# Performance work log

Hardware: AMD Instinct MI355X
Metric: run time of the kernel (lower is better)

## Reference

```python
import jax, jax.numpy as jnp
import numpy as np

HEADS = 4
PK = 32  # patch_kernel


def _starts(size, step, d):
    out = []
    for i in range(0, size + step - d, step):
        out.append(min(i, size - d))
    return np.asarray(out)


def dwconv3(x, w, b=None):
    # depthwise 3x3 conv, NCHW, weight (C,1,3,3)
    y = jax.lax.conv_general_dilated(
        x, w, window_strides=(1, 1), padding=((1, 1), (1, 1)),
        dimension_numbers=("NCHW", "OIHW", "NCHW"), feature_group_count=x.shape[1])
    if b is not None:
        y = y + b[None, :, None, None]
    return y


def conv1(x, w):
    # 1x1 conv as channel matmul, weight (O, C)
    return jnp.einsum("bchw,oc->bohw", x, w)


def partition(x, step, d):
    # overlapping windows, matching local_partition (i outer, j inner)
    b, c, h, w = x.shape
    sh = _starts(h, step, d)
    sw = _starts(w, step, d)
    ridx = sh[:, None] + np.arange(d)            # (nh, d)
    cidx = sw[:, None] + np.arange(d)            # (nw, d)
    xw = x[:, :, ridx, :]                        # (b, c, nh, d, w)
    xw = xw[:, :, :, :, cidx]                    # (b, c, nh, d, nw, d)
    xw = jnp.transpose(xw, (0, 2, 4, 1, 3, 5))   # (b, nh, nw, c, d, d)
    return xw.reshape(b, len(sh) * len(sw), c, d, d)


def reverse(shape, win, step, d):
    # overlap-add + count-based averaging, matching local_reverse
    b, c, h, w = shape
    sh = _starts(h, step, d)
    sw = _starts(w, step, d)
    nh, nw = len(sh), len(sw)
    ridx = (sh[:, None] + np.arange(d)).reshape(nh, 1, d, 1)
    cidx = (sw[:, None] + np.arange(d)).reshape(1, nw, 1, d)
    win6 = win.reshape(b, nh, nw, c, d, d).transpose(0, 3, 1, 2, 4, 5)  # (b,c,nh,nw,d,d)
    out = jnp.zeros(shape, win.dtype).at[:, :, ridx, cidx].add(win6)
    cnt = jnp.zeros((h, w), win.dtype).at[ridx, cidx].add(1.0)
    return out / cnt[None, None]


def setup_inputs() -> dict:
    key = jax.random.key(0)
    ks = jax.random.split(key, 9)
    b, dim, Hs, Hx = 2, 128, 62, 248
    s = 0.05
    return {
        "x": jax.random.normal(ks[0], (b, dim, Hx, Hx), jnp.float32),
        "sp": jax.random.normal(ks[1], (b, dim, Hs, Hs), jnp.float32),
        "w_pos": jax.random.normal(ks[2], (dim, 1, 3, 3), jnp.float32) * s,
        "b_pos": jax.random.normal(ks[3], (dim,), jnp.float32) * s,
        "w_q": jax.random.normal(ks[4], (dim, dim), jnp.float32) * s,
        "w_qdw": jax.random.normal(ks[5], (dim, 1, 3, 3), jnp.float32) * s,
        "w_kv": jax.random.normal(ks[6], (2 * dim, dim), jnp.float32) * s,
        "w_kvdw": jax.random.normal(ks[7], (2 * dim, 1, 3, 3), jnp.float32) * s,
        "w_out": jax.random.normal(ks[8], (dim, dim), jnp.float32) * s,
    }


def reference(x, sp, w_pos, b_pos, w_q, w_qdw, w_kv, w_kvdw, w_out):
    p1, p2 = PK, PK // 4               # 32, 8
    s1, s2 = p1 - p1 // 4, p2 - p2 // 4  # 24, 6
    x = x + dwconv3(x, w_pos, b_pos)
    sp = sp + dwconv3(sp, w_pos, b_pos)
    q = dwconv3(conv1(sp, w_q), w_qdw)      # (b, c, Hs, Ws)
    kv = dwconv3(conv1(x, w_kv), w_kvdw)    # (b, 2c, Hx, Wx)
    qw = partition(q, s2, p2)               # (b, n, c, 8, 8)
    kvw = partition(kv, s1, p1)             # (b, n, 2c, 32, 32)
    kw, vw = jnp.split(kvw, 2, axis=2)
    b, n, c = qw.shape[0], qw.shape[1], qw.shape[2]
    hd = c // HEADS

    def to_heads(t, d):  # 'b n (head c) dh dw -> (b n) head (dh dw) c'
        return t.reshape(b * n, HEADS, hd, d * d).transpose(0, 1, 3, 2)

    qh, kh, vh = to_heads(qw, p2), to_heads(kw, p1), to_heads(vw, p1)
    attn = jax.nn.softmax(jnp.einsum("bhqc,bhkc->bhqk", qh, kh) * (hd ** -0.5), axis=-1)
    out = jnp.einsum("bhqk,bhkc->bhqc", attn, vh)
    out = out.transpose(0, 1, 3, 2).reshape(b, n, c, p2, p2)
    out = reverse(sp.shape, out, s2, p2)
    return conv1(out, w_out)
```

## Files before the change

kernel.cpp:

```cpp
#include <hip/hip_runtime.h>
#include <cstdint>

#define HS 62
#define HX 248
#define HXW (HX * HX)
#define HSW (HS * HS)
#define HXP 256
#define HXWP (HX * HXP)

typedef __attribute__((ext_vector_type(8))) short bf16x8;
typedef __attribute__((ext_vector_type(4))) float f32x4;
typedef __attribute__((ext_vector_type(2))) float f32x2;

static __device__ __forceinline__ unsigned short f2bf(float f) {
  uint32_t u = __builtin_bit_cast(uint32_t, f);
  u += 0x7fff + ((u >> 16) & 1);
  return (unsigned short)(u >> 16);
}
static __device__ __forceinline__ float bf2f(unsigned short u) {
  uint32_t x = (uint32_t)u << 16;
  return __builtin_bit_cast(float, x);
}
static __device__ __forceinline__ float bflo(uint32_t u) {
  return __builtin_bit_cast(float, u << 16);
}
static __device__ __forceinline__ float bfhi(uint32_t u) {
  return __builtin_bit_cast(float, u & 0xffff0000u);
}

static __device__ __forceinline__ void pkfma(f32x2& acc, f32x2 a, f32x2 b) {
  asm("v_pk_fma_f32 %0, %1, %2, %0" : "+v"(acc) : "v"(a), "v"(b));
}
static __device__ __forceinline__ uint32_t cvtpk(float lo, float hi) {
  uint32_t r;
  asm("v_cvt_pk_bf16_f32 %0, %1, %2" : "=v"(r) : "v"(lo), "v"(hi));
  return r;
}
static __device__ __forceinline__ f32x2 unp(uint32_t u) {
  f32x2 r;
  r.x = __builtin_bit_cast(float, u << 16);
  r.y = __builtin_bit_cast(float, u & 0xffff0000u);
  return r;
}

__global__ void dwconv3_kernel(const float* __restrict__ x, const float* __restrict__ w,
                               const float* __restrict__ bias, float* __restrict__ y,
                               int C, int H, int W, int total, int residual) {
  int i = blockIdx.x * 256 + threadIdx.x;
  if (i >= total) return;
  int wx = i % W;
  int t = i / W;
  int hy = t % H;
  int bc = t / H;
  int c = bc % C;
  const float* xb = x + (size_t)bc * H * W;
  const float* wc = w + c * 9;
  float s = bias ? bias[c] : 0.0f;
  for (int di = -1; di <= 1; di++) {
    int h2 = hy + di;
    if (h2 < 0 || h2 >= H) continue;
    for (int dj = -1; dj <= 1; dj++) {
      int w2 = wx + dj;
      if (w2 < 0 || w2 >= W) continue;
      s += xb[(size_t)h2 * W + w2] * wc[(di + 1) * 3 + (dj + 1)];
    }
  }
  if (residual) s += xb[(size_t)hy * W + wx];
  y[i] = s;
}

__global__ __launch_bounds__(256) void dwconv8x2_bf16_kernel(
    const float* __restrict__ x, const float* __restrict__ w,
    const float* __restrict__ bias, unsigned short* __restrict__ y, int total) {
  int i = blockIdx.x * 256 + threadIdx.x;
  if (i >= total) return;
  int wq = (i % 31) * 8;
  int t = i / 31;
  int hp = t % 124;
  int bc = t / 124;
  int c = bc & 127;
  int hy = hp * 2;
  const float* xb = x + (size_t)bc * HXW;
  const float* wc = w + c * 9;
  float bv = bias[c];

  float rm1[10], r0[10], r1[10], r2[10];
  auto loadrow = [&](int h2, float (&r)[10]) {
    const float* row = xb + (size_t)h2 * HX + wq;
    float4 a = *(const float4*)row;
    float4 b2 = *(const float4*)(row + 4);
    r[1] = a.x;  r[2] = a.y;  r[3] = a.z;  r[4] = a.w;
    r[5] = b2.x; r[6] = b2.y; r[7] = b2.z; r[8] = b2.w;
    r[0] = (wq > 0) ? row[-1] : 0.0f;
    r[9] = (wq + 8 < HX) ? row[8] : 0.0f;
  };
  loadrow((hy > 0) ? hy - 1 : 0, rm1);
  loadrow(hy, r0);
  loadrow(hy + 1, r1);
  loadrow((hy + 2 < HX) ? hy + 2 : HX - 1, r2);
  if (hp == 0) {
#pragma unroll
    for (int k = 0; k < 10; k++) rm1[k] = 0.0f;
  }
  if (hp == 123) {
#pragma unroll
    for (int k = 0; k < 10; k++) r2[k] = 0.0f;
  }

  float w0 = wc[0], w1 = wc[1], w2 = wc[2];
  float w3 = wc[3], w4 = wc[4], w5 = wc[5];
  float w6 = wc[6], w7 = wc[7], w8 = wc[8];

  float o0[8], o1[8];
#pragma unroll
  for (int k = 0; k < 8; k++) {
    float s = bv;
    s += w0 * rm1[k]; s += w1 * rm1[k + 1]; s += w2 * rm1[k + 2];
    s += w3 * r0[k];  s += w4 * r0[k + 1];  s += w5 * r0[k + 2];
    s += w6 * r1[k];  s += w7 * r1[k + 1];  s += w8 * r1[k + 2];
    o0[k] = s + r0[k + 1];
    float u = bv;
    u += w0 * r0[k]; u += w1 * r0[k + 1]; u += w2 * r0[k + 2];
    u += w3 * r1[k]; u += w4 * r1[k + 1]; u += w5 * r1[k + 2];
    u += w6 * r2[k]; u += w7 * r2[k + 1]; u += w8 * r2[k + 2];
    o1[k] = u + r1[k + 1];
  }
  uint4 d0, d1;
  d0.x = cvtpk(o0[0], o0[1]); d0.y = cvtpk(o0[2], o0[3]);
  d0.z = cvtpk(o0[4], o0[5]); d0.w = cvtpk(o0[6], o0[7]);
  d1.x = cvtpk(o1[0], o1[1]); d1.y = cvtpk(o1[2], o1[3]);
  d1.z = cvtpk(o1[4], o1[5]); d1.w = cvtpk(o1[6], o1[7]);
  unsigned short* yb = y + (size_t)bc * HXW + (size_t)hy * HX + wq;
  *(uint4*)yb = d0;
  *(uint4*)(yb + HX) = d1;
}

__global__ void cvt_bf16_kernel(const float* __restrict__ src, unsigned short* __restrict__ dst,
                                int n) {
  int i = blockIdx.x * 256 + threadIdx.x;
  if (i < n) dst[i] = f2bf(src[i]);
}

__global__ void dwconv_q_kernel(const float* __restrict__ x, const float* __restrict__ w,
                                unsigned short* __restrict__ qn, int total) {
  int i = blockIdx.x * 256 + threadIdx.x;
  if (i >= total) return;
  int wx = i % HS;
  int t = i / HS;
  int hy = t % HS;
  int bc = t / HS;
  int c = bc & 127;
  int b = bc >> 7;
  const float* xb = x + (size_t)bc * HSW;
  const float* wc = w + c * 9;
  float s = 0.0f;
  for (int di = -1; di <= 1; di++) {
    int h2 = hy + di;
    if (h2 < 0 || h2 >= HS) continue;
    for (int dj = -1; dj <= 1; dj++) {
      int w2 = wx + dj;
      if (w2 < 0 || w2 >= HS) continue;
      s += xb[(size_t)h2 * HS + w2] * wc[(di + 1) * 3 + (dj + 1)];
    }
  }
  qn[((size_t)(b * HSW + hy * HS + wx)) * 128 + c] = f2bf(s * 0.17677669529663688f);
}

__global__ __launch_bounds__(256) void conv1_kv_mfma_kernel(
    const unsigned short* __restrict__ xpb,
    const unsigned short* __restrict__ wkb,
    unsigned short* __restrict__ y) {
  int b = blockIdx.y;
  int p0 = blockIdx.x * 64;
  int tid = threadIdx.x;
  int wave = tid >> 6, lane = tid & 63, quad = lane >> 4, l15 = lane & 15;
  __shared__ __align__(16) unsigned short bufA[64 * 136];
  __shared__ __align__(16) unsigned short bufW[64 * 136];

  {
    int c = tid >> 1, half = tid & 1;
    const unsigned short* src = xpb + ((size_t)(b * 128 + c)) * HXW + p0 + half * 32;
#pragma unroll
    for (int j = 0; j < 8; j++) {
      uint2 v = *(const uint2*)(src + j * 4);
      int px = half * 32 + j * 4;
      bufA[(px + 0) * 136 + c] = (unsigned short)(v.x & 0xffff);
      bufA[(px + 1) * 136 + c] = (unsigned short)(v.x >> 16);
      bufA[(px + 2) * 136 + c] = (unsigned short)(v.y & 0xffff);
      bufA[(px + 3) * 136 + c] = (unsigned short)(v.y >> 16);
    }
  }
  __syncthreads();
  bf16x8 A[4];
#pragma unroll
  for (int kb = 0; kb < 4; kb++)
    A[kb] = __builtin_bit_cast(bf16x8,
        *(const uint4*)&bufA[(wave * 16 + l15) * 136 + kb * 32 + quad * 8]);

  const f32x4 zf = {0.f, 0.f, 0.f, 0.f};
#pragma unroll 1
  for (int h = 0; h < 2; h++) {
#pragma unroll 1
    for (int oq = 0; oq < 2; oq++) {
      __syncthreads();
      {
        int orow = tid >> 2;
        int cseg = (tid & 3) * 32;
        const unsigned short* src = wkb + (size_t)(h * 128 + oq * 64 + orow) * 128 + cseg;
        unsigned short* dst = &bufW[orow * 136 + cseg];
        *(uint4*)(dst)      = *(const uint4*)(src);
        *(uint4*)(dst + 8)  = *(const uint4*)(src + 8);
        *(uint4*)(dst + 16) = *(const uint4*)(src + 16);
        *(uint4*)(dst + 24) = *(const uint4*)(src + 24);
      }
      __syncthreads();
#pragma unroll
      for (int ot = 0; ot < 4; ot++) {
        const unsigned short* wrow = &bufW[(ot * 16 + l15) * 136 + quad * 8];
        f32x4 D = zf;
        D = __builtin_amdgcn_mfma_f32_16x16x32_bf16(A[0], __builtin_bit_cast(bf16x8, *(const uint4*)(wrow)),      D, 0, 0, 0);
        D = __builtin_amdgcn_mfma_f32_16x16x32_bf16(A[1], __builtin_bit_cast(bf16x8, *(const uint4*)(wrow + 32)), D, 0, 0, 0);
        D = __builtin_amdgcn_mfma_f32_16x16x32_bf16(A[2], __builtin_bit_cast(bf16x8, *(const uint4*)(wrow + 64)), D, 0, 0, 0);
        D = __builtin_amdgcn_mfma_f32_16x16x32_bf16(A[3], __builtin_bit_cast(bf16x8, *(const uint4*)(wrow + 96)), D, 0, 0, 0);
#pragma unroll
        for (int r = 0; r < 4; r++)
          bufA[(wave * 16 + quad * 4 + r) * 136 + (oq * 4 + ot) * 16 + l15] = f2bf(D[r]);
      }
    }
    __syncthreads();
    {
      int px = tid >> 2, og = (tid & 3) * 32;
      const uint4* srcp = (const uint4*)&bufA[px * 136 + og];
      uint4* dstp = (uint4*)(y + ((size_t)b * HXW + p0 + px) * 256 + h * 128 + og);
#pragma unroll
      for (int j = 0; j < 4; j++) dstp[j] = srcp[j];
    }
  }
}

template <bool VT, bool VB>
static __device__ __forceinline__ void dwkv_rowpair(
    const unsigned short* __restrict__ rm1, const unsigned short* __restrict__ r0,
    const unsigned short* __restrict__ r1, const unsigned short* __restrict__ r2,
    const f32x2 (&wp)[9], int px0, f32x2 (&a0)[8], f32x2 (&a1)[8]) {
  const f32x2 z2 = {0.f, 0.f};
#pragma unroll
  for (int p = 0; p < 8; p++) { a0[p] = z2; a1[p] = z2; }
#pragma unroll
  for (int j = 0; j < 10; j++) {
    int xcol = px0 - 1 + j;
    int xc = xcol;
    if (j == 0) xc = (xcol < 0) ? 0 : xcol;
    if (j == 9) xc = (xcol > HX - 1) ? HX - 1 : xcol;
    size_t off = (size_t)xc * 256;
    uint32_t um1 = 0, u0, u1, u2 = 0;
    u0 = *(const uint32_t*)(r0 + off);
    u1 = *(const uint32_t*)(r1 + off);
    if constexpr (VT) um1 = *(const uint32_t*)(rm1 + off);
    if constexpr (VB) u2 = *(const uint32_t*)(r2 + off);
    if (j == 0 || j == 9) {
      bool oob = (j == 0) ? (xcol < 0) : (xcol > HX - 1);
      if (oob) { um1 = 0u; u0 = 0u; u1 = 0u; u2 = 0u; }
    }
    f32x2 dm1, d0 = unp(u0), d1 = unp(u1), d2;
    if constexpr (VT) dm1 = unp(um1);
    if constexpr (VB) d2 = unp(u2);
    if (j <= 7) {
      if constexpr (VT) pkfma(a0[j], wp[0], dm1);
      pkfma(a0[j], wp[3], d0);
      pkfma(a0[j], wp[6], d1);
      pkfma(a1[j], wp[0], d0);
      pkfma(a1[j], wp[3], d1);
      if constexpr (VB) pkfma(a1[j], wp[6], d2);
    }
    if (j >= 1 && j <= 8) {
      if constexpr (VT) pkfma(a0[j - 1], wp[1], dm1);
      pkfma(a0[j - 1], wp[4], d0);
      pkfma(a0[j - 1], wp[7], d1);
      pkfma(a1[j - 1], wp[1], d0);
      pkfma(a1[j - 1], wp[4], d1);
      if constexpr (VB) pkfma(a1[j - 1], wp[7], d2);
    }
    if (j >= 2) {
      if constexpr (VT) pkfma(a0[j - 2], wp[2], dm1);
      pkfma(a0[j - 2], wp[5], d0);
      pkfma(a0[j - 2], wp[8], d1);
      pkfma(a1[j - 2], wp[2], d0);
      pkfma(a1[j - 2], wp[5], d1);
      if constexpr (VB) pkfma(a1[j - 2], wp[8], d2);
    }
  }
}

#define VTS 72
#define VTROW (128 * VTS + 16)

__global__ __launch_bounds__(512) __attribute__((amdgpu_waves_per_eu(4)))
void dwconv_kv_kernel(const unsigned short* __restrict__ tkv,
                      const float* __restrict__ w,
                      unsigned short* __restrict__ kT,
                      unsigned short* __restrict__ vv) {
  int fid = blockIdx.x;
  int xcd = fid & 7, slot = fid >> 3;
  int gi = xcd * 62 + slot;
  int strip = gi / 124;
  int g = gi % 124;
  int b = blockIdx.y;
  int x0 = strip * 64;
  int tid = threadIdx.x;
  int cl = tid & 127;
  int pg = tid >> 7;
  int ch0 = cl * 2;
  int hy0 = g * 2;

  f32x2 wp[9];
#pragma unroll
  for (int t = 0; t < 9; t++) {
    wp[t].x = w[ch0 * 9 + t];
    wp[t].y = w[(ch0 + 1) * 9 + t];
  }

  __shared__ __align__(16) unsigned short vt[2 * VTROW];

  const unsigned short* r0 = tkv + (size_t)b * HXW * 256 + (size_t)hy0 * (HX * 256) + ch0;
  const unsigned short* r1 = r0 + HX * 256;
  const unsigned short* rm1 = r0 - HX * 256;
  const unsigned short* r2 = r1 + HX * 256;
  bool isK = (cl < 64);
  int c0 = ch0 - 128;

#pragma unroll 1
  for (int half = 0; half < 2; half++) {
    int px0 = x0 + pg * 16 + half * 8;
    if (px0 < HX) {
      f32x2 a0[8], a1[8];
      if (g == 0)        dwkv_rowpair<false, true >(rm1, r0, r1, r2, wp, px0, a0, a1);
      else if (g == 123) dwkv_rowpair<true,  false>(rm1, r0, r1, r2, wp, px0, a0, a1);
      else               dwkv_rowpair<true,  true >(rm1, r0, r1, r2, wp, px0, a0, a1);

      if (isK) {
        unsigned short* kb0 = kT + ((size_t)b * HXW + (size_t)hy0 * HX + px0) * 128 + ch0;
        unsigned short* kb1 = kb0 + (size_t)HX * 128;
#pragma unroll
        for (int p = 0; p < 8; p++) {
          *(uint32_t*)(kb0 + (size_t)p * 128) = cvtpk(a0[p].x, a0[p].y);
          *(uint32_t*)(kb1 + (size_t)p * 128) = cvtpk(a1[p].x, a1[p].y);
        }
      } else {
        int pxr = pg * 16 + half * 8;
        unsigned short* v0 = vt + c0 * VTS + pxr;
        unsigned short* v1 = v0 + VTS;
        uint2 d;
        d.x = cvtpk(a0[0].x, a0[1].x); d.y = cvtpk(a0[2].x, a0[3].x);
        *(uint2*)(v0) = d;
        d.x = cvtpk(a0[4].x, a0[5].x); d.y = cvtpk(a0[6].x, a0[7].x);
        *(uint2*)(v0 + 4) = d;
        d.x = cvtpk(a0[0].y, a0[1].y); d.y = cvtpk(a0[2].y, a0[3].y);
        *(uint2*)(v1) = d;
        d.x = cvtpk(a0[4].y, a0[5].y); d.y = cvtpk(a0[6].y, a0[7].y);
        *(uint2*)(v1 + 4) = d;
        d.x = cvtpk(a1[0].x, a1[1].x); d.y = cvtpk(a1[2].x, a1[3].x);
        *(uint2*)(v0 + VTROW) = d;
        d.x = cvtpk(a1[4].x, a1[5].x); d.y = cvtpk(a1[6].x, a1[7].x);
        *(uint2*)(v0 + VTROW + 4) = d;
        d.x = cvtpk(a1[0].y, a1[1].y); d.y = cvtpk(a1[2].y, a1[3].y);
        *(uint2*)(v1 + VTROW) = d;
        d.x = cvtpk(a1[4].y, a1[5].y); d.y = cvtpk(a1[6].y, a1[7].y);
        *(uint2*)(v1 + VTROW + 4) = d;
      }
    }
  }
  __syncthreads();
  {
    int ch = tid >> 2;
    int row = (tid >> 1) & 1;
    int ph = (tid & 1) * 32;
    const unsigned short* srcv = vt + row * VTROW + ch * VTS + ph;
    unsigned short* dst = vv + (size_t)(b * 128 + ch) * HXWP + (size_t)(hy0 + row) * HXP + x0 + ph;
#pragma unroll
    for (int j = 0; j < 4; j++)
      *(uint4*)(dst + j * 8) = *(const uint4*)(srcv + j * 8);
  }
}

template <int O>
__global__ __launch_bounds__(256) void conv1_kernel(const float* __restrict__ x,
                                                    const float* __restrict__ w,
                                                    float* __restrict__ y, int HW) {
  constexpr int K = 128;
  constexpr int BK = 32;
  __shared__ __align__(16) float ws_s[BK][64];
  __shared__ __align__(16) float xs_s[BK][64];
  int b = blockIdx.z;
  int o0 = blockIdx.y * 64;
  int p0 = blockIdx.x * 64;
  const float* xb = x + (size_t)b * K * HW;
  int tx = threadIdx.x & 15;
  int ty = threadIdx.x >> 4;
  float acc[4][4] = {};
  int lo = threadIdx.x >> 2;
  int lk = (threadIdx.x & 3) * 8;
  int lc = threadIdx.x >> 3;
  int lp = (threadIdx.x & 7) * 8;

  for (int k0 = 0; k0 < K; k0 += BK) {
    __syncthreads();
    {
      const float* wp = w + (size_t)(o0 + lo) * K + k0 + lk;
      float4 a = *(const float4*)wp;
      float4 bq = *(const float4*)(wp + 4);
      ws_s[lk + 0][lo] = a.x;  ws_s[lk + 1][lo] = a.y;
      ws_s[lk + 2][lo] = a.z;  ws_s[lk + 3][lo] = a.w;
      ws_s[lk + 4][lo] = bq.x; ws_s[lk + 5][lo] = bq.y;
      ws_s[lk + 6][lo] = bq.z; ws_s[lk + 7][lo] = bq.w;
    }
    {
      int p = p0 + lp;
      const float* xp = xb + (size_t)(k0 + lc) * HW;
      float4 a, bq;
      if (p + 7 < HW) {
        a = *(const float4*)(xp + p);
        bq = *(const float4*)(xp + p + 4);
      } else {
        float tv[8];
#pragma unroll
        for (int j = 0; j < 8; j++) tv[j] = (p + j < HW) ? xp[p + j] : 0.0f;
        a = make_float4(tv[0], tv[1], tv[2], tv[3]);
        bq = make_float4(tv[4], tv[5], tv[6], tv[7]);
      }
      *(float4*)&xs_s[lc][lp] = a;
      *(float4*)&xs_s[lc][lp + 4] = bq;
    }
    __syncthreads();
#pragma unroll
    for (int k = 0; k < BK; k++) {
      float4 wv = *(const float4*)&ws_s[k][ty * 4];
      float4 xv = *(const float4*)&xs_s[k][tx * 4];
      acc[0][0] += wv.x * xv.x; acc[0][1] += wv.x * xv.y; acc[0][2] += wv.x * xv.z; acc[0][3] += wv.x * xv.w;
      acc[1][0] += wv.y * xv.x; acc[1][1] += wv.y * xv.y; acc[1][2] += wv.y * xv.z; acc[1][3] += wv.y * xv.w;
      acc[2][0] += wv.z * xv.x; acc[2][1] += wv.z * xv.y; acc[2][2] += wv.z * xv.z; acc[2][3] += wv.z * xv.w;
      acc[3][0] += wv.w * xv.x; acc[3][1] += wv.w * xv.y; acc[3][2] += wv.w * xv.z; acc[3][3] += wv.w * xv.w;
    }
  }
  int p = p0 + tx * 4;
  float* yb = y + (size_t)b * O * HW + (size_t)(o0 + ty * 4) * HW;
#pragma unroll
  for (int j = 0; j < 4; j++) {
    float* yr = yb + (size_t)j * HW + p;
    if (p + 3 < HW) {
      *(float4*)yr = make_float4(acc[j][0], acc[j][1], acc[j][2], acc[j][3]);
    } else {
#pragma unroll
      for (int e = 0; e < 4; e++) if (p + e < HW) yr[e] = acc[j][e];
    }
  }
}

__global__ __launch_bounds__(512) void attn_mfma_kernel(
    const unsigned short* __restrict__ qn,
    const unsigned short* __restrict__ kT,
    const unsigned short* __restrict__ vp,
    float* __restrict__ o) {
  int n = blockIdx.x, hp = blockIdx.y, b = blockIdx.z;
  int wi = n / 10, wj = n % 10;
  int wave = threadIdx.x >> 6;
  int hd = wave & 1, oct = wave >> 1;
  int h = hp * 2 + hd;
  int lane = threadIdx.x & 63;
  int quad = lane >> 4;
  int l15 = lane & 15;
  int y0 = 24 * wi, x0 = 24 * wj;

  __shared__ __align__(16) unsigned short lds[20480];
  unsigned short* Pw = lds + wave * 2560;

  bf16x8 QB[4];
#pragma unroll
  for (int nt = 0; nt < 4; nt++) {
    int qq = nt * 16 + l15;
    int qy = 6 * wi + (qq >> 3), qx = 6 * wj + (qq & 7);
    QB[nt] = __builtin_bit_cast(bf16x8,
        *(const uint4*)(qn + ((size_t)(b * HSW + qy * HS + qx)) * 128 + h * 32 + quad * 8));
  }

  f32x4 Oacc[2][4];
#pragma unroll
  for (int a = 0; a < 2; a++)
#pragma unroll
    for (int c = 0; c < 4; c++) Oacc[a][c] = f32x4{0.f, 0.f, 0.f, 0.f};
  float lsum[4] = {0.f, 0.f, 0.f, 0.f};

  const unsigned short* kb = kT + (size_t)b * HXW * 128 + h * 32;
  const unsigned short* vb = vp + ((size_t)(b * 128 + h * 32)) * HXWP;
  const f32x4 zf = {0.f, 0.f, 0.f, 0.f};

#define LOADROW(r, K0, K1, V0, V1)                                              \
  {                                                                             \
    int y = y0 + (r);                                                           \
    const unsigned short* krow = kb + ((size_t)(y * HX + x0)) * 128;            \
    K0 = *(const uint4*)(krow + (size_t)l15 * 128 + quad * 8);                  \
    K1 = *(const uint4*)(krow + (size_t)(16 + l15) * 128 + quad * 8);           \
    const unsigned short* vrow = vb + (size_t)y * HXP + x0 + quad * 8;          \
    V0 = *(const uint4*)(vrow + (size_t)l15 * HXWP);                            \
    V1 = *(const uint4*)(vrow + (size_t)(16 + l15) * HXWP);                     \
  }

  auto compute = [&](uint4 k0, uint4 k1, uint4 v0, uint4 v1) {
    bf16x8 KA0 = __builtin_bit_cast(bf16x8, k0);
    bf16x8 KA1 = __builtin_bit_cast(bf16x8, k1);
    bf16x8 VA0 = __builtin_bit_cast(bf16x8, v0);
    bf16x8 VA1 = __builtin_bit_cast(bf16x8, v1);
    f32x4 S[2][4];
#pragma unroll
    for (int nt = 0; nt < 4; nt++) {
      S[0][nt] = __builtin_amdgcn_mfma_f32_16x16x32_bf16(KA0, QB[nt], zf, 0, 0, 0);
      S[1][nt] = __builtin_amdgcn_mfma_f32_16x16x32_bf16(KA1, QB[nt], zf, 0, 0, 0);
    }
#pragma unroll
    for (int nt = 0; nt < 4; nt++) {
      float pv[2][4];
      float cs = 0.f;
#pragma unroll
      for (int mt = 0; mt < 2; mt++)
#pragma unroll
        for (int r = 0; r < 4; r++) {
          pv[mt][r] = __expf(S[mt][nt][r]);
          cs += pv[mt][r];
        }
      lsum[nt] += cs;
#pragma unroll
      for (int mt = 0; mt < 2; mt++) {
        uint2 d;
        d.x = (uint32_t)f2bf(pv[mt][0]) | ((uint32_t)f2bf(pv[mt][1]) << 16);
        d.y = (uint32_t)f2bf(pv[mt][2]) | ((uint32_t)f2bf(pv[mt][3]) << 16);
        *(uint2*)(Pw + (16 * nt + l15) * 40 + 16 * mt + quad * 4) = d;
      }
    }
#pragma unroll
    for (int nt = 0; nt < 4; nt++) {
      bf16x8 PB = __builtin_bit_cast(bf16x8, *(const uint4*)(Pw + (16 * nt + l15) * 40 + quad * 8));
      Oacc[0][nt] = __builtin_amdgcn_mfma_f32_16x16x32_bf16(VA0, PB, Oacc[0][nt], 0, 0, 0);
      Oacc[1][nt] = __builtin_amdgcn_mfma_f32_16x16x32_bf16(VA1, PB, Oacc[1][nt], 0, 0, 0);
    }
  };

  int rbase = oct * 8;
  uint4 kA0, kA1, vA0, vA1, kB0, kB1, vB0, vB1;
  LOADROW(rbase + 0, kA0, kA1, vA0, vA1);
  LOADROW(rbase + 1, kB0, kB1, vB0, vB1);
#pragma unroll 1
  for (int r = 0; r < 8; r += 2) {
    compute(kA0, kA1, vA0, vA1);
    {
      int rn = (r + 2 < 8) ? (r + 2) : 6;
      LOADROW(rbase + rn, kA0, kA1, vA0, vA1);
    }
    compute(kB0, kB1, vB0, vB1);
    {
      int rn = (r + 3 < 8) ? (r + 3) : 7;
      LOADROW(rbase + rn, kB0, kB1, vB0, vB1);
    }
  }
#undef LOADROW

#pragma unroll
  for (int nt = 0; nt < 4; nt++) {
    lsum[nt] += __shfl_xor(lsum[nt], 16, 64);
    lsum[nt] += __shfl_xor(lsum[nt], 32, 64);
  }

  float* mO = (float*)lds;
  float* mL = (float*)(lds + 16384);
#pragma unroll 1
  for (int p = 0; p < 2; p++) {
    __syncthreads();
    if (hd == p) {
#pragma unroll
      for (int mt = 0; mt < 2; mt++)
#pragma unroll
        for (int nt = 0; nt < 4; nt++)
#pragma unroll
          for (int r = 0; r < 4; r++)
            mO[oct * 2048 + (16 * mt + quad * 4 + r) * 64 + 16 * nt + l15] = Oacc[mt][nt][r];
      if (quad == 0) {
#pragma unroll
        for (int nt = 0; nt < 4; nt++) mL[oct * 64 + nt * 16 + l15] = lsum[nt];
      }
    }
    __syncthreads();
    {
      int q = threadIdx.x & 63;
      int cg = threadIdx.x >> 6;
      float inv = 1.0f / (mL[q] + mL[64 + q] + mL[128 + q] + mL[192 + q]);
      float* ob = o + (((size_t)(b * 100 + n)) * 128 + (hp * 2 + p) * 32 + cg * 4) * 64 + q;
#pragma unroll
      for (int e = 0; e < 4; e++) {
        int ch = cg * 4 + e;
        float s = mO[ch * 64 + q] + mO[2048 + ch * 64 + q] +
                  mO[4096 + ch * 64 + q] + mO[6144 + ch * 64 + q];
        ob[(size_t)e * 64] = s * inv;
      }
    }
  }
}

__global__ void reverse_kernel(const float* __restrict__ win, float* __restrict__ out) {
  int i = blockIdx.x * 256 + threadIdx.x;
  const int total = 2 * 128 * HSW;
  if (i >= total) return;
  int x = i % HS;
  int t = i / HS;
  int y = t % HS;
  t /= HS;
  int c = t % 128;
  int b = t / 128;
  int wi0 = (y >= 7) ? (y - 2) / 6 : 0;
  int wi1 = min(9, y / 6);
  int wj0 = (x >= 7) ? (x - 2) / 6 : 0;
  int wj1 = min(9, x / 6);
  float s = 0.0f;
  for (int wi = wi0; wi <= wi1; wi++)
    for (int wj = wj0; wj <= wj1; wj++) {
      int di = y - 6 * wi, dj = x - 6 * wj;
      s += win[(((size_t)(b * 100 + wi * 10 + wj)) * 128 + c) * 64 + di * 8 + dj];
    }
  float cnt = (float)((wi1 - wi0 + 1) * (wj1 - wj0 + 1));
  out[i] = s / cnt;
}

extern "C" void kernel_launch(void* const* d_in, const int* in_sizes, int n_in,
                              void* d_out, int out_size, void* d_ws, size_t ws_size,
                              hipStream_t stream) {
  const float* x      = (const float*)d_in[0];
  const float* sp     = (const float*)d_in[1];
  const float* w_pos  = (const float*)d_in[2];
  const float* b_pos  = (const float*)d_in[3];
  const float* w_q    = (const float*)d_in[4];
  const float* w_qdw  = (const float*)d_in[5];
  const float* w_kv   = (const float*)d_in[6];
  const float* w_kvdw = (const float*)d_in[7];
  const float* w_out  = (const float*)d_in[8];
  float* out = (float*)d_out;

  const size_t N_x   = (size_t)2 * 128 * HXW;
  const size_t N_vp  = (size_t)2 * 128 * HXWP;
  const size_t N_s   = (size_t)2 * 128 * HSW;
  const size_t N_att = (size_t)2 * 100 * 128 * 64;

  float* ws = (float*)d_ws;
  unsigned short* xpb = (unsigned short*)ws;
  unsigned short* kT  = (unsigned short*)ws;
  unsigned short* vv  = kT + N_x;
  unsigned short* tkv = vv + N_vp;
  float* att = (float*)tkv;
  float* rev = att + N_att;
  float* spp = (float*)(tkv + 2 * N_x);
  float* tq  = spp + N_s;
  unsigned short* qn  = (unsigned short*)(tq + N_s);
  unsigned short* wkb = qn + N_s;
  (void)ws_size; (void)in_sizes; (void)n_in; (void)out_size;

  cvt_bf16_kernel<<<128, 256, 0, stream>>>(w_kv, wkb, 256 * 128);
  {
    int total = 2 * 128 * 124 * 31;
    dwconv8x2_bf16_kernel<<<(total + 255) / 256, 256, 0, stream>>>(x, w_pos, b_pos, xpb, total);
  }
  {
    int total = (int)N_s;
    dwconv3_kernel<<<(total + 255) / 256, 256, 0, stream>>>(sp, w_pos, b_pos, spp, 128, HS, HS, total, 1);
  }
  {
    int HW = HSW;
    dim3 grid((HW + 63) / 64, 2, 2);
    conv1_kernel<128><<<grid, 256, 0, stream>>>(spp, w_q, tq, HW);
  }
  {
    int total = (int)N_s;
    dwconv_q_kernel<<<(total + 255) / 256, 256, 0, stream>>>(tq, w_qdw, qn, total);
  }
  {
    dim3 grid(HXW / 64, 2);
    conv1_kv_mfma_kernel<<<grid, 256, 0, stream>>>(xpb, wkb, tkv);
  }
  {
    dim3 grid(496, 2);
    dwconv_kv_kernel<<<grid, 512, 0, stream>>>(tkv, w_kvdw, kT, vv);
  }
  {
    dim3 grid(100, 2, 2);
    attn_mfma_kernel<<<grid, 512, 0, stream>>>(qn, kT, vv, att);
  }
  {
    int total = (int)N_s;
    reverse_kernel<<<(total + 255) / 256, 256, 0, stream>>>(att, rev);
  }
  {
    int HW = HSW;
    dim3 grid((HW + 63) / 64, 2, 2);
    conv1_kernel<128><<<grid, 256, 0, stream>>>(rev, w_out, out, HW);
  }
}
```

Before: 269.6 us.

## Split attention key rows across two blocks with combine pass and XCD-aware block mapping

The attention kernel grid doubles from 400 to 800 blocks by splitting the 32 key rows of each window into two halves. Each block writes unnormalized partial outputs and partial softmax sums to workspace, and a new combine kernel adds the two halves and normalizes. Block indices are also remapped so consecutive IDs spread across the XCDs while blocks on the same XCD share windows. The aim is better GPU occupancy and cache locality, at the cost of an extra kernel launch and extra global traffic for the partials. The combine step relies on softmax using no max subtraction, so the partial sums add directly.

```diff
diff --git a/kernel.cpp b/kernel.cpp
--- a/kernel.cpp
+++ b/kernel.cpp
@@ -460,8 +460,14 @@
     const unsigned short* __restrict__ qn,
     const unsigned short* __restrict__ kT,
     const unsigned short* __restrict__ vp,
-    float* __restrict__ o) {
-  int n = blockIdx.x, hp = blockIdx.y, b = blockIdx.z;
+    float* __restrict__ pO,
+    float* __restrict__ pL) {
+  int fid = blockIdx.x;
+  int xcd = fid & 7, slot = fid >> 3;
+  int lin = xcd * 100 + slot;
+  int n = lin % 100;
+  int g2 = lin / 100;
+  int half = g2 & 1, hp = (g2 >> 1) & 1, b = g2 >> 2;
   int wi = n / 10, wj = n % 10;
   int wave = threadIdx.x >> 6;
   int hd = wave & 1, oct = wave >> 1;
@@ -544,23 +550,16 @@
     }
   };
 
-  int rbase = oct * 8;
+  int rbase = half * 16 + oct * 4;
   uint4 kA0, kA1, vA0, vA1, kB0, kB1, vB0, vB1;
   LOADROW(rbase + 0, kA0, kA1, vA0, vA1);
   LOADROW(rbase + 1, kB0, kB1, vB0, vB1);
-#pragma unroll 1
-  for (int r = 0; r < 8; r += 2) {
-    compute(kA0, kA1, vA0, vA1);
-    {
-      int rn = (r + 2 < 8) ? (r + 2) : 6;
-      LOADROW(rbase + rn, kA0, kA1, vA0, vA1);
-    }
-    compute(kB0, kB1, vB0, vB1);
-    {
-      int rn = (r + 3 < 8) ? (r + 3) : 7;
-      LOADROW(rbase + rn, kB0, kB1, vB0, vB1);
-    }
-  }
+  compute(kA0, kA1, vA0, vA1);
+  LOADROW(rbase + 2, kA0, kA1, vA0, vA1);
+  compute(kB0, kB1, vB0, vB1);
+  LOADROW(rbase + 3, kB0, kB1, vB0, vB1);
+  compute(kA0, kA1, vA0, vA1);
+  compute(kB0, kB1, vB0, vB1);
 #undef LOADROW
 
 #pragma unroll
@@ -591,17 +590,36 @@
     {
       int q = threadIdx.x & 63;
       int cg = threadIdx.x >> 6;
-      float inv = 1.0f / (mL[q] + mL[64 + q] + mL[128 + q] + mL[192 + q]);
-      float* ob = o + (((size_t)(b * 100 + n)) * 128 + (hp * 2 + p) * 32 + cg * 4) * 64 + q;
+      float Lh = mL[q] + mL[64 + q] + mL[128 + q] + mL[192 + q];
+      size_t pbase = ((((size_t)(b * 100 + n)) * 4 + (hp * 2 + p)) * 2 + half);
+      float* ob = pO + pbase * 2048 + (size_t)(cg * 4) * 64 + q;
 #pragma unroll
       for (int e = 0; e < 4; e++) {
         int ch = cg * 4 + e;
         float s = mO[ch * 64 + q] + mO[2048 + ch * 64 + q] +
                   mO[4096 + ch * 64 + q] + mO[6144 + ch * 64 + q];
-        ob[(size_t)e * 64] = s * inv;
+        ob[(size_t)e * 64] = s;
       }
-    }
-  }
+      if (cg == 0) pL[pbase * 64 + q] = Lh;
+    }
+  }
+}
+
+__global__ void attn_combine_kernel(const float* __restrict__ pO,
+                                    const float* __restrict__ pL,
+                                    float* __restrict__ o) {
+  int i = blockIdx.x * 256 + threadIdx.x;
+  const int total = 2 * 100 * 128 * 64;
+  if (i >= total) return;
+  int q = i & 63;
+  int t = i >> 6;
+  int c = t & 127;
+  int wn = t >> 7;
+  int head = c >> 5, ch = c & 31;
+  size_t base = ((size_t)wn * 4 + head) * 2;
+  float s = pO[(base + 0) * 2048 + ch * 64 + q] + pO[(base + 1) * 2048 + ch * 64 + q];
+  float L = pL[(base + 0) * 64 + q] + pL[(base + 1) * 64 + q];
+  o[i] = s / L;
 }
 
 __global__ void reverse_kernel(const float* __restrict__ win, float* __restrict__ out) {
@@ -646,6 +664,8 @@
   const size_t N_vp  = (size_t)2 * 128 * HXWP;
   const size_t N_s   = (size_t)2 * 128 * HSW;
   const size_t N_att = (size_t)2 * 100 * 128 * 64;
+  const size_t N_pO  = (size_t)2 * 100 * 4 * 2 * 2048;
+  const size_t N_pL  = (size_t)2 * 100 * 4 * 2 * 64;
 
   float* ws = (float*)d_ws;
   unsigned short* xpb = (unsigned short*)ws;
@@ -654,6 +674,8 @@
   unsigned short* tkv = vv + N_vp;
   float* att = (float*)tkv;
   float* rev = att + N_att;
+  float* pO  = rev + N_s;
+  float* pL  = pO + N_pO;
   float* spp = (float*)(tkv + 2 * N_x);
   float* tq  = spp + N_s;
   unsigned short* qn  = (unsigned short*)(tq + N_s);
@@ -687,8 +709,11 @@
     dwconv_kv_kernel<<<grid, 512, 0, stream>>>(tkv, w_kvdw, kT, vv);
   }
   {
-    dim3 grid(100, 2, 2);
-    attn_mfma_kernel<<<grid, 512, 0, stream>>>(qn, kT, vv, att);
+    attn_mfma_kernel<<<800, 512, 0, stream>>>(qn, kT, vv, pO, pL);
+  }
+  {
+    int total = (int)N_att;
+    attn_combine_kernel<<<(total + 255) / 256, 256, 0, stream>>>(pO, pL, att);
   }
   {
     int total = (int)N_s;
```

New measurement: 268.6 us. About the same (-0.4%).
